# Performance work log

Hardware: AMD Instinct MI355X
Metric: run time of the kernel (lower is better)

Reference implementation:

```python
import jax, jax.numpy as jnp
import numpy as np

N_TH1 = 25
LB = 1e-20
UB = 1e20
LB_EXP = -20.0


def _make_directions(n_th1):
    # Spherical direction grid exactly as in the TF __init__ (interior ring points, then 2 poles).
    n_th2 = 2 * (n_th1 - 1) + 1
    th1 = np.linspace(-np.pi / 2, np.pi / 2, n_th1)
    th2 = np.linspace(-np.pi, np.pi, n_th2)
    c1, s1 = np.cos(th1), np.sin(th1)
    c2, s2 = np.cos(th2), np.sin(th2)
    i = np.arange(1, n_th1 - 1)
    j = np.arange(0, n_th2 - 1)
    C1 = c1[i][:, None]
    dx = (C1 * c2[j][None, :]).ravel()
    dy = (C1 * s2[j][None, :]).ravel()
    dz = np.broadcast_to(s1[i][:, None], (len(i), len(j))).ravel()
    d = np.stack([dx, dy, dz], axis=-1)
    poles = np.array([[c1[0] * c2[0], c1[0] * s2[0], s1[0]],
                      [c1[-1] * c2[0], c1[-1] * s2[0], s1[-1]]])
    return np.concatenate([d, poles], axis=0).astype(np.float32)  # [n_dirs, 3]


def setup_inputs():
    key = jax.random.key(0)
    k1, k2 = jax.random.split(key)
    B, P, V = 8, 32, 256
    vertices = jax.random.normal(k1, (B, P, V, 3), dtype=jnp.float32)
    # smoothness p in [2, 20] (power-mean exponent must be > 1 for meaningful support fn)
    smoothness = jax.random.uniform(k2, (B, P), dtype=jnp.float32) * 18.0 + 2.0
    directions = jnp.asarray(_make_directions(N_TH1))  # [1106, 3]
    return {"vertices": vertices, "smoothness": smoothness, "directions": directions}


def _forward(vertices, smoothness, directions):
    B, P, V, _ = vertices.shape
    D = directions.shape[0]
    mean_vertices = jnp.mean(vertices, axis=2, keepdims=True)          # [B,P,1,3]
    local_vertices = vertices - mean_vertices                          # [B,P,V,3]

    # z[b,p,v,d] = <local_vertex, direction>
    z = jnp.einsum('bpvc,dc->bpvd', local_vertices, directions)        # [B,P,V,D]
    zm = jnp.where(z > 0, z, 0.0)                                      # relu, == cast(z>0)*z
    p = smoothness[:, :, None, None]                                   # [B,P,1,1]

    # dynamic rescaling exponent k = 10^ceil(max(0, (-20 - p*log10(max_v zm)) / p))
    safe_zm = jnp.where(zm > 0, zm, 1.0)
    zm_log = jnp.max(jnp.where(zm > 0, jnp.log(safe_zm) / jnp.log(10.0), -jnp.inf),
                     axis=2, keepdims=True)                            # [B,P,1,D]
    exponent = zm_log * p
    lk = jnp.where(exponent < LB_EXP, (LB_EXP - exponent) / p, 0.0)
    k = jnp.power(10.0, jnp.clip(jnp.ceil(lk), 0.0, UB))               # [B,P,1,D]
    k = jax.lax.stop_gradient(k)  # ceil has zero grad in TF too

    zms = zm * k                                                       # [B,P,V,D]
    # zm^p, with exact-zero entries mapped back to 0 (clip(0^p)=LB then -LB in TF)
    safe_zms = jnp.where(zms > 0, zms, 1.0)
    zm_p = jnp.where(zms > 0, jnp.clip(jnp.power(safe_zms, p), LB, UB), 0.0)
    sum_zm_p = jnp.sum(zm_p, axis=2, keepdims=True)                    # [B,P,1,D]
    h = jnp.clip(jnp.power(sum_zm_p, 1.0 / p), LB, UB)                 # [B,P,1,D]

    # dh/dz = clip((zm_scaled / h)^(p-1)); TF keeps the LB floor here (no subtraction)
    ratio = zms / h
    safe_ratio = jnp.where(ratio > 0, ratio, 1.0)
    dhdz = jnp.where(ratio > 0, jnp.clip(jnp.power(safe_ratio, p - 1.0), LB, UB), LB)

    # surface points s = (dh/dz)^T V + t
    surf = jnp.einsum('bpvd,bpvc->bpdc', dhdz, local_vertices) + mean_vertices  # [B,P,D,3]

    h_out = jnp.transpose(h / k, (0, 1, 3, 2))                         # [B,P,D,1]
    local_dirs = jnp.broadcast_to(directions[None, None], (B, P, D, 3))
    direction_h = jnp.concatenate([local_dirs, h_out], axis=-1)        # [B,P,D,4]

    points = surf.reshape(B, P * D, 3)
    mean_v = mean_vertices.reshape(B, P, 3)
    zeros = jnp.zeros((1, 1, 1, 1), jnp.float32)
    return (points, direction_h, mean_v, directions, local_vertices, zeros, zeros)


def reference(vertices, smoothness, directions):
    return _forward(vertices, smoothness, directions)
```

## Files before the change

### kernel.cpp

```cpp
#include <hip/hip_runtime.h>
#include <math.h>

#define BLOCK 256
#define LBv 1e-20f
#define UBv 1e20f
#define LOG10_2 0.3010299956639812f

#if __has_builtin(__builtin_amdgcn_logf) && __has_builtin(__builtin_amdgcn_exp2f)
__device__ __forceinline__ float fast_log2(float x) { return __builtin_amdgcn_logf(x); }
__device__ __forceinline__ float fast_exp2(float x) { return __builtin_amdgcn_exp2f(x); }
#else
__device__ __forceinline__ float fast_log2(float x) { return log2f(x); }
__device__ __forceinline__ float fast_exp2(float x) { return exp2f(x); }
#endif

__global__ __launch_bounds__(BLOCK) void mcnet_fused(
    const float* __restrict__ verts,
    const float* __restrict__ smooth,
    const float* __restrict__ dirs,
    float* __restrict__ out,
    int NT, int V, int D, int SPLIT,
    size_t offDH, size_t offMV, size_t offDIR, size_t offLV, size_t offZ)
{
    extern __shared__ float smem[];
    float4* lv = (float4*)smem;
    float*  red = smem + 4 * (size_t)V;

    const int tid  = threadIdx.x;
    const int tile = blockIdx.x / SPLIT;
    const int s    = blockIdx.x % SPLIT;

    float sx = 0.f, sy = 0.f, sz = 0.f;
    for (int v = tid; v < V; v += BLOCK) {
        const float* vp = verts + ((size_t)tile * V + v) * 3;
        sx += vp[0]; sy += vp[1]; sz += vp[2];
    }
    red[tid] = sx; red[tid + BLOCK] = sy; red[tid + 2 * BLOCK] = sz;
    __syncthreads();
    for (int st = BLOCK / 2; st > 0; st >>= 1) {
        if (tid < st) {
            red[tid]             += red[tid + st];
            red[tid + BLOCK]     += red[tid + BLOCK + st];
            red[tid + 2 * BLOCK] += red[tid + 2 * BLOCK + st];
        }
        __syncthreads();
    }
    const float inv = 1.0f / (float)V;
    const float mx = red[0] * inv, my = red[BLOCK] * inv, mz = red[2 * BLOCK] * inv;

    for (int v = tid; v < V; v += BLOCK) {
        const float* vp = verts + ((size_t)tile * V + v) * 3;
        lv[v] = make_float4(vp[0] - mx, vp[1] - my, vp[2] - mz, 0.f);
    }
    __syncthreads();

    if (s == 0) {
        for (int v = tid; v < V; v += BLOCK) {
            float4 q = lv[v];
            size_t o = offLV + ((size_t)tile * V + v) * 3;
            out[o + 0] = q.x;
            out[o + 1] = q.y;
            out[o + 2] = q.z;
        }
        if (tid == 0) {
            size_t mo = offMV + (size_t)tile * 3;
            out[mo + 0] = mx;
            out[mo + 1] = my;
            out[mo + 2] = mz;
        }
    }
    if (blockIdx.x == 0) {
        for (int i = tid; i < D * 3; i += BLOCK)
            out[offDIR + i] = dirs[i];
        if (tid < 2) out[offZ + tid] = 0.f;
    }

    const int d = s * BLOCK + tid;
    if (d >= D) return;

    const float dx = dirs[d * 3 + 0];
    const float dy = dirs[d * 3 + 1];
    const float dz = dirs[d * 3 + 2];
    const float pv = smooth[tile];
    const float c1 = pv - 1.f;

    float zmax = 0.f, S = 0.f;
    float ax = 0.f, ay = 0.f, az = 0.f;
    #pragma unroll 8
    for (int v = 0; v < V; ++v) {
        float4 q = lv[v];
        float z  = fmaf(q.x, dx, fmaf(q.y, dy, q.z * dz));
        float zc = fmaxf(z, 0.f);
        zmax = fmaxf(zmax, zc);
        float l = fast_log2(zc);
        float w = fast_exp2(c1 * l);
        float u = w * zc;
        S += fminf(u, UBv);
        ax = fmaf(w, q.x, ax);
        ay = fmaf(w, q.y, ay);
        az = fmaf(w, q.z, az);
    }

    if (zmax > 0.f && pv * (fast_log2(zmax) * LOG10_2) >= -10.f) {
        float h = fminf(fmaxf(fast_exp2(fast_log2(S) * (1.f / pv)), LBv), UBv);
        float scale = fast_exp2(-c1 * fast_log2(h));

        size_t po = ((size_t)tile * D + d) * 3;
        out[po + 0] = fmaf(ax, scale, mx);
        out[po + 1] = fmaf(ay, scale, my);
        out[po + 2] = fmaf(az, scale, mz);

        size_t dho = offDH + ((size_t)tile * D + d) * 4;
        out[dho + 0] = dx;
        out[dho + 1] = dy;
        out[dho + 2] = dz;
        out[dho + 3] = h;
    } else {
        float zm_log   = (zmax > 0.f) ? log10f(zmax) : -INFINITY;
        float exponent = zm_log * pv;
        float lk = (exponent < -20.f) ? (-20.f - exponent) / pv : 0.f;
        float kk = powf(10.f, fminf(fmaxf(ceilf(lk), 0.f), UBv));

        float sum = 0.f;
        for (int v = 0; v < V; ++v) {
            float4 q = lv[v];
            float z   = fmaf(q.x, dx, fmaf(q.y, dy, q.z * dz));
            float zms = fmaxf(z, 0.f) * kk;
            float w   = (zms > 0.f) ? fminf(fmaxf(powf(zms, pv), LBv), UBv) : 0.f;
            sum += w;
        }
        float h = fminf(fmaxf(powf(sum, 1.f / pv), LBv), UBv);

        float bx = 0.f, by = 0.f, bz = 0.f;
        for (int v = 0; v < V; ++v) {
            float4 q = lv[v];
            float z     = fmaf(q.x, dx, fmaf(q.y, dy, q.z * dz));
            float zms   = fmaxf(z, 0.f) * kk;
            float ratio = zms / h;
            float w = (ratio > 0.f) ? fminf(fmaxf(powf(ratio, c1), LBv), UBv) : LBv;
            bx = fmaf(w, q.x, bx);
            by = fmaf(w, q.y, by);
            bz = fmaf(w, q.z, bz);
        }

        size_t po = ((size_t)tile * D + d) * 3;
        out[po + 0] = bx + mx;
        out[po + 1] = by + my;
        out[po + 2] = bz + mz;

        size_t dho = offDH + ((size_t)tile * D + d) * 4;
        out[dho + 0] = dx;
        out[dho + 1] = dy;
        out[dho + 2] = dz;
        out[dho + 3] = h / kk;
    }
}

extern "C" void kernel_launch(void* const* d_in, const int* in_sizes, int n_in,
                              void* d_out, int out_size, void* d_ws, size_t ws_size,
                              hipStream_t stream) {
    const float* verts  = (const float*)d_in[0];
    const float* smooth = (const float*)d_in[1];
    const float* dirs   = (const float*)d_in[2];
    float* out = (float*)d_out;

    const int NT = in_sizes[1];
    const int D  = in_sizes[2] / 3;
    const int V  = in_sizes[0] / (3 * NT);
    const int SPLIT = (D + BLOCK - 1) / BLOCK;

    const size_t offDH  = (size_t)NT * D * 3;
    const size_t offMV  = offDH  + (size_t)NT * D * 4;
    const size_t offDIR = offMV  + (size_t)NT * 3;
    const size_t offLV  = offDIR + (size_t)D * 3;
    const size_t offZ   = offLV  + (size_t)NT * V * 3;

    const size_t shmem = (4 * (size_t)V + 3 * BLOCK) * sizeof(float);

    dim3 grid(NT * SPLIT);
    dim3 block(BLOCK);
    hipLaunchKernelGGL(mcnet_fused, grid, block, shmem, stream,
                       verts, smooth, dirs, out,
                       NT, V, D, SPLIT, offDH, offMV, offDIR, offLV, offZ);
}
```

Before: 92.90 us.

## Process two directions per thread and drop per-vertex max tracking

Each thread now computes two directions at once, so every shared-memory vertex load is reused across both, and the grid shrinks from five splits per tile to three. The per-vertex zmax tracking and UB clamp in the hot loop are removed. The decision to take the fast path now tests the accumulated sum against a threshold, and zmax is recomputed only on the slow path. This cuts LDS traffic and instructions per direction but lowers occupancy and parallelism (fewer blocks, and the second direction idles on the last split), and the branch condition changes numerically.

Measured after the change: 97.32 us. 1.05x slower.

```diff
diff --git a/kernel.cpp b/kernel.cpp
--- a/kernel.cpp
+++ b/kernel.cpp
@@ -4,7 +4,6 @@
 #define BLOCK 256
 #define LBv 1e-20f
 #define UBv 1e20f
-#define LOG10_2 0.3010299956639812f
 
 #if __has_builtin(__builtin_amdgcn_logf) && __has_builtin(__builtin_amdgcn_exp2f)
 __device__ __forceinline__ float fast_log2(float x) { return __builtin_amdgcn_logf(x); }
@@ -14,7 +13,70 @@
 __device__ __forceinline__ float fast_exp2(float x) { return exp2f(x); }
 #endif
 
-__global__ __launch_bounds__(BLOCK) void mcnet_fused(
+__device__ __forceinline__ void finish_dir(
+    const float4* __restrict__ lv, int V, int tile, int d, int D,
+    float dx, float dy, float dz, float pv, float c1,
+    float S, float ax, float ay, float az,
+    float mx, float my, float mz, float Sthresh,
+    float* __restrict__ out, size_t offDH)
+{
+    size_t po  = ((size_t)tile * D + d) * 3;
+    size_t dho = offDH + ((size_t)tile * D + d) * 4;
+
+    if (S >= Sthresh) {
+        float h = fminf(fmaxf(fast_exp2(fast_log2(S) * (1.f / pv)), LBv), UBv);
+        float scale = fast_exp2(-c1 * fast_log2(h));
+        out[po + 0] = fmaf(ax, scale, mx);
+        out[po + 1] = fmaf(ay, scale, my);
+        out[po + 2] = fmaf(az, scale, mz);
+        out[dho + 0] = dx;
+        out[dho + 1] = dy;
+        out[dho + 2] = dz;
+        out[dho + 3] = h;
+    } else {
+        float zmax = 0.f;
+        for (int v = 0; v < V; ++v) {
+            float4 q = lv[v];
+            float z = fmaf(q.x, dx, fmaf(q.y, dy, q.z * dz));
+            zmax = fmaxf(zmax, z);
+        }
+        float zm_log   = (zmax > 0.f) ? log10f(zmax) : -INFINITY;
+        float exponent = zm_log * pv;
+        float lk = (exponent < -20.f) ? (-20.f - exponent) / pv : 0.f;
+        float kk = powf(10.f, fminf(fmaxf(ceilf(lk), 0.f), UBv));
+
+        float sum = 0.f;
+        for (int v = 0; v < V; ++v) {
+            float4 q = lv[v];
+            float z   = fmaf(q.x, dx, fmaf(q.y, dy, q.z * dz));
+            float zms = fmaxf(z, 0.f) * kk;
+            float w   = (zms > 0.f) ? fminf(fmaxf(powf(zms, pv), LBv), UBv) : 0.f;
+            sum += w;
+        }
+        float h = fminf(fmaxf(powf(sum, 1.f / pv), LBv), UBv);
+
+        float bx = 0.f, by = 0.f, bz = 0.f;
+        for (int v = 0; v < V; ++v) {
+            float4 q = lv[v];
+            float z     = fmaf(q.x, dx, fmaf(q.y, dy, q.z * dz));
+            float zms   = fmaxf(z, 0.f) * kk;
+            float ratio = zms / h;
+            float w = (ratio > 0.f) ? fminf(fmaxf(powf(ratio, c1), LBv), UBv) : LBv;
+            bx = fmaf(w, q.x, bx);
+            by = fmaf(w, q.y, by);
+            bz = fmaf(w, q.z, bz);
+        }
+        out[po + 0] = bx + mx;
+        out[po + 1] = by + my;
+        out[po + 2] = bz + mz;
+        out[dho + 0] = dx;
+        out[dho + 1] = dy;
+        out[dho + 2] = dz;
+        out[dho + 3] = h / kk;
+    }
+}
+
+__global__ __launch_bounds__(BLOCK) void mcnet_fused2(
     const float* __restrict__ verts,
     const float* __restrict__ smooth,
     const float* __restrict__ dirs,
@@ -75,85 +137,47 @@
         if (tid < 2) out[offZ + tid] = 0.f;
     }
 
-    const int d = s * BLOCK + tid;
-    if (d >= D) return;
-
-    const float dx = dirs[d * 3 + 0];
-    const float dy = dirs[d * 3 + 1];
-    const float dz = dirs[d * 3 + 2];
+    const int d0 = s * (2 * BLOCK) + tid;
+    if (d0 >= D) return;
+    const int d1 = d0 + BLOCK;
+    const bool has1 = (d1 < D);
+    const int d1c = has1 ? d1 : d0;
+
+    const float dx0 = dirs[d0 * 3 + 0], dy0 = dirs[d0 * 3 + 1], dz0 = dirs[d0 * 3 + 2];
+    const float dx1 = dirs[d1c * 3 + 0], dy1 = dirs[d1c * 3 + 1], dz1 = dirs[d1c * 3 + 2];
     const float pv = smooth[tile];
     const float c1 = pv - 1.f;
-
-    float zmax = 0.f, S = 0.f;
-    float ax = 0.f, ay = 0.f, az = 0.f;
-    #pragma unroll 8
+    const float Sthresh = (float)V * 1e-10f;
+
+    float S0 = 0.f, ax0 = 0.f, ay0 = 0.f, az0 = 0.f;
+    float S1 = 0.f, ax1 = 0.f, ay1 = 0.f, az1 = 0.f;
+
+    #pragma unroll 4
     for (int v = 0; v < V; ++v) {
         float4 q = lv[v];
-        float z  = fmaf(q.x, dx, fmaf(q.y, dy, q.z * dz));
-        float zc = fmaxf(z, 0.f);
-        zmax = fmaxf(zmax, zc);
-        float l = fast_log2(zc);
-        float w = fast_exp2(c1 * l);
-        float u = w * zc;
-        S += fminf(u, UBv);
-        ax = fmaf(w, q.x, ax);
-        ay = fmaf(w, q.y, ay);
-        az = fmaf(w, q.z, az);
-    }
-
-    if (zmax > 0.f && pv * (fast_log2(zmax) * LOG10_2) >= -10.f) {
-        float h = fminf(fmaxf(fast_exp2(fast_log2(S) * (1.f / pv)), LBv), UBv);
-        float scale = fast_exp2(-c1 * fast_log2(h));
-
-        size_t po = ((size_t)tile * D + d) * 3;
-        out[po + 0] = fmaf(ax, scale, mx);
-        out[po + 1] = fmaf(ay, scale, my);
-        out[po + 2] = fmaf(az, scale, mz);
-
-        size_t dho = offDH + ((size_t)tile * D + d) * 4;
-        out[dho + 0] = dx;
-        out[dho + 1] = dy;
-        out[dho + 2] = dz;
-        out[dho + 3] = h;
-    } else {
-        float zm_log   = (zmax > 0.f) ? log10f(zmax) : -INFINITY;
-        float exponent = zm_log * pv;
-        float lk = (exponent < -20.f) ? (-20.f - exponent) / pv : 0.f;
-        float kk = powf(10.f, fminf(fmaxf(ceilf(lk), 0.f), UBv));
-
-        float sum = 0.f;
-        for (int v = 0; v < V; ++v) {
-            float4 q = lv[v];
-            float z   = fmaf(q.x, dx, fmaf(q.y, dy, q.z * dz));
-            float zms = fmaxf(z, 0.f) * kk;
-            float w   = (zms > 0.f) ? fminf(fmaxf(powf(zms, pv), LBv), UBv) : 0.f;
-            sum += w;
-        }
-        float h = fminf(fmaxf(powf(sum, 1.f / pv), LBv), UBv);
-
-        float bx = 0.f, by = 0.f, bz = 0.f;
-        for (int v = 0; v < V; ++v) {
-            float4 q = lv[v];
-            float z     = fmaf(q.x, dx, fmaf(q.y, dy, q.z * dz));
-            float zms   = fmaxf(z, 0.f) * kk;
-            float ratio = zms / h;
-            float w = (ratio > 0.f) ? fminf(fmaxf(powf(ratio, c1), LBv), UBv) : LBv;
-            bx = fmaf(w, q.x, bx);
-            by = fmaf(w, q.y, by);
-            bz = fmaf(w, q.z, bz);
-        }
-
-        size_t po = ((size_t)tile * D + d) * 3;
-        out[po + 0] = bx + mx;
-        out[po + 1] = by + my;
-        out[po + 2] = bz + mz;
-
-        size_t dho = offDH + ((size_t)tile * D + d) * 4;
-        out[dho + 0] = dx;
-        out[dho + 1] = dy;
-        out[dho + 2] = dz;
-        out[dho + 3] = h / kk;
-    }
+        float z0 = fmaf(q.x, dx0, fmaf(q.y, dy0, q.z * dz0));
+        float z1 = fmaf(q.x, dx1, fmaf(q.y, dy1, q.z * dz1));
+        float zc0 = fmaxf(z0, 0.f);
+        float zc1 = fmaxf(z1, 0.f);
+        float l0 = fast_log2(zc0);
+        float l1 = fast_log2(zc1);
+        float w0 = fast_exp2(c1 * l0);
+        float w1 = fast_exp2(c1 * l1);
+        S0 = fmaf(w0, zc0, S0);
+        S1 = fmaf(w1, zc1, S1);
+        ax0 = fmaf(w0, q.x, ax0);
+        ay0 = fmaf(w0, q.y, ay0);
+        az0 = fmaf(w0, q.z, az0);
+        ax1 = fmaf(w1, q.x, ax1);
+        ay1 = fmaf(w1, q.y, ay1);
+        az1 = fmaf(w1, q.z, az1);
+    }
+
+    finish_dir(lv, V, tile, d0, D, dx0, dy0, dz0, pv, c1,
+               S0, ax0, ay0, az0, mx, my, mz, Sthresh, out, offDH);
+    if (has1)
+        finish_dir(lv, V, tile, d1, D, dx1, dy1, dz1, pv, c1,
+                   S1, ax1, ay1, az1, mx, my, mz, Sthresh, out, offDH);
 }
 
 extern "C" void kernel_launch(void* const* d_in, const int* in_sizes, int n_in,
@@ -167,7 +191,7 @@
     const int NT = in_sizes[1];
     const int D  = in_sizes[2] / 3;
     const int V  = in_sizes[0] / (3 * NT);
-    const int SPLIT = (D + BLOCK - 1) / BLOCK;
+    const int SPLIT = (D + 2 * BLOCK - 1) / (2 * BLOCK);
 
     const size_t offDH  = (size_t)NT * D * 3;
     const size_t offMV  = offDH  + (size_t)NT * D * 4;
@@ -179,7 +203,7 @@
 
     dim3 grid(NT * SPLIT);
     dim3 block(BLOCK);
-    hipLaunchKernelGGL(mcnet_fused, grid, block, shmem, stream,
+    hipLaunchKernelGGL(mcnet_fused2, grid, block, shmem, stream,
                        verts, smooth, dirs, out,
                        NT, V, D, SPLIT, offDH, offMV, offDIR, offLV, offZ);
 }
```

## Read vertices via uniform global loads and fold mean subtraction algebraically

Applied to the files above, without the earlier changes.

The main loop now reads raw vertices straight from global memory with block-uniform addresses, which the compiler can turn into scalar loads, instead of staging centered vertices in LDS. The mean is folded into the dot product as a constant offset, and a running weight sum Ws corrects the weighted vertex sums afterwards. The per-vertex zmax tracking and the UB clamp are dropped, and the fast-path test becomes a threshold on S instead of on zmax. This trims LDS traffic and per-iteration ALU work, at the cost of a slightly different fast/slow path criterion and possible cancellation error in the mean correction.

After: 91.80 us. Within noise of the previous version (-1.2%).

```diff
diff --git a/kernel.cpp b/kernel.cpp
--- a/kernel.cpp
+++ b/kernel.cpp
@@ -4,7 +4,6 @@
 #define BLOCK 256
 #define LBv 1e-20f
 #define UBv 1e20f
-#define LOG10_2 0.3010299956639812f
 
 #if __has_builtin(__builtin_amdgcn_logf) && __has_builtin(__builtin_amdgcn_exp2f)
 __device__ __forceinline__ float fast_log2(float x) { return __builtin_amdgcn_logf(x); }
@@ -14,7 +13,7 @@
 __device__ __forceinline__ float fast_exp2(float x) { return exp2f(x); }
 #endif
 
-__global__ __launch_bounds__(BLOCK) void mcnet_fused(
+__global__ __launch_bounds__(BLOCK) void mcnet_sreg(
     const float* __restrict__ verts,
     const float* __restrict__ smooth,
     const float* __restrict__ dirs,
@@ -22,18 +21,17 @@
     int NT, int V, int D, int SPLIT,
     size_t offDH, size_t offMV, size_t offDIR, size_t offLV, size_t offZ)
 {
-    extern __shared__ float smem[];
-    float4* lv = (float4*)smem;
-    float*  red = smem + 4 * (size_t)V;
+    __shared__ float red[3 * BLOCK];
 
     const int tid  = threadIdx.x;
     const int tile = blockIdx.x / SPLIT;
     const int s    = blockIdx.x % SPLIT;
 
+    const float* vp0 = verts + (size_t)tile * V * 3;
+
     float sx = 0.f, sy = 0.f, sz = 0.f;
     for (int v = tid; v < V; v += BLOCK) {
-        const float* vp = verts + ((size_t)tile * V + v) * 3;
-        sx += vp[0]; sy += vp[1]; sz += vp[2];
+        sx += vp0[3 * v + 0]; sy += vp0[3 * v + 1]; sz += vp0[3 * v + 2];
     }
     red[tid] = sx; red[tid + BLOCK] = sy; red[tid + 2 * BLOCK] = sz;
     __syncthreads();
@@ -48,19 +46,12 @@
     const float inv = 1.0f / (float)V;
     const float mx = red[0] * inv, my = red[BLOCK] * inv, mz = red[2 * BLOCK] * inv;
 
-    for (int v = tid; v < V; v += BLOCK) {
-        const float* vp = verts + ((size_t)tile * V + v) * 3;
-        lv[v] = make_float4(vp[0] - mx, vp[1] - my, vp[2] - mz, 0.f);
-    }
-    __syncthreads();
-
     if (s == 0) {
         for (int v = tid; v < V; v += BLOCK) {
-            float4 q = lv[v];
             size_t o = offLV + ((size_t)tile * V + v) * 3;
-            out[o + 0] = q.x;
-            out[o + 1] = q.y;
-            out[o + 2] = q.z;
+            out[o + 0] = vp0[3 * v + 0] - mx;
+            out[o + 1] = vp0[3 * v + 1] - my;
+            out[o + 2] = vp0[3 * v + 2] - mz;
         }
         if (tid == 0) {
             size_t mo = offMV + (size_t)tile * 3;
@@ -83,39 +74,50 @@
     const float dz = dirs[d * 3 + 2];
     const float pv = smooth[tile];
     const float c1 = pv - 1.f;
+    const float Sthresh = (float)V * 1e-10f;
 
-    float zmax = 0.f, S = 0.f;
-    float ax = 0.f, ay = 0.f, az = 0.f;
+    const float nmd = -(mx * dx + my * dy + mz * dz);
+
+    float S = 0.f, Wx = 0.f, Wy = 0.f, Wz = 0.f, Ws = 0.f;
     #pragma unroll 8
     for (int v = 0; v < V; ++v) {
-        float4 q = lv[v];
-        float z  = fmaf(q.x, dx, fmaf(q.y, dy, q.z * dz));
+        float vx = vp0[3 * v + 0];
+        float vy = vp0[3 * v + 1];
+        float vz = vp0[3 * v + 2];
+        float z  = fmaf(vx, dx, fmaf(vy, dy, fmaf(vz, dz, nmd)));
         float zc = fmaxf(z, 0.f);
-        zmax = fmaxf(zmax, zc);
-        float l = fast_log2(zc);
-        float w = fast_exp2(c1 * l);
-        float u = w * zc;
-        S += fminf(u, UBv);
-        ax = fmaf(w, q.x, ax);
-        ay = fmaf(w, q.y, ay);
-        az = fmaf(w, q.z, az);
+        float l  = fast_log2(zc);
+        float w  = fast_exp2(c1 * l);
+        S  = fmaf(w, zc, S);
+        Wx = fmaf(w, vx, Wx);
+        Wy = fmaf(w, vy, Wy);
+        Wz = fmaf(w, vz, Wz);
+        Ws += w;
     }
 
-    if (zmax > 0.f && pv * (fast_log2(zmax) * LOG10_2) >= -10.f) {
+    size_t po  = ((size_t)tile * D + d) * 3;
+    size_t dho = offDH + ((size_t)tile * D + d) * 4;
+
+    if (S >= Sthresh) {
         float h = fminf(fmaxf(fast_exp2(fast_log2(S) * (1.f / pv)), LBv), UBv);
         float scale = fast_exp2(-c1 * fast_log2(h));
-
-        size_t po = ((size_t)tile * D + d) * 3;
+        float ax = fmaf(-mx, Ws, Wx);
+        float ay = fmaf(-my, Ws, Wy);
+        float az = fmaf(-mz, Ws, Wz);
         out[po + 0] = fmaf(ax, scale, mx);
         out[po + 1] = fmaf(ay, scale, my);
         out[po + 2] = fmaf(az, scale, mz);
-
-        size_t dho = offDH + ((size_t)tile * D + d) * 4;
         out[dho + 0] = dx;
         out[dho + 1] = dy;
         out[dho + 2] = dz;
         out[dho + 3] = h;
     } else {
+        float zmax = 0.f;
+        for (int v = 0; v < V; ++v) {
+            float z = fmaf(vp0[3 * v] - mx, dx,
+                      fmaf(vp0[3 * v + 1] - my, dy, (vp0[3 * v + 2] - mz) * dz));
+            zmax = fmaxf(zmax, z);
+        }
         float zm_log   = (zmax > 0.f) ? log10f(zmax) : -INFINITY;
         float exponent = zm_log * pv;
         float lk = (exponent < -20.f) ? (-20.f - exponent) / pv : 0.f;
@@ -123,8 +125,8 @@
 
         float sum = 0.f;
         for (int v = 0; v < V; ++v) {
-            float4 q = lv[v];
-            float z   = fmaf(q.x, dx, fmaf(q.y, dy, q.z * dz));
+            float z = fmaf(vp0[3 * v] - mx, dx,
+                      fmaf(vp0[3 * v + 1] - my, dy, (vp0[3 * v + 2] - mz) * dz));
             float zms = fmaxf(z, 0.f) * kk;
             float w   = (zms > 0.f) ? fminf(fmaxf(powf(zms, pv), LBv), UBv) : 0.f;
             sum += w;
@@ -133,22 +135,18 @@
 
         float bx = 0.f, by = 0.f, bz = 0.f;
         for (int v = 0; v < V; ++v) {
-            float4 q = lv[v];
-            float z     = fmaf(q.x, dx, fmaf(q.y, dy, q.z * dz));
+            float lx = vp0[3 * v] - mx, ly = vp0[3 * v + 1] - my, lz = vp0[3 * v + 2] - mz;
+            float z     = fmaf(lx, dx, fmaf(ly, dy, lz * dz));
             float zms   = fmaxf(z, 0.f) * kk;
             float ratio = zms / h;
             float w = (ratio > 0.f) ? fminf(fmaxf(powf(ratio, c1), LBv), UBv) : LBv;
-            bx = fmaf(w, q.x, bx);
-            by = fmaf(w, q.y, by);
-            bz = fmaf(w, q.z, bz);
+            bx = fmaf(w, lx, bx);
+            by = fmaf(w, ly, by);
+            bz = fmaf(w, lz, bz);
         }
-
-        size_t po = ((size_t)tile * D + d) * 3;
         out[po + 0] = bx + mx;
         out[po + 1] = by + my;
         out[po + 2] = bz + mz;
-
-        size_t dho = offDH + ((size_t)tile * D + d) * 4;
         out[dho + 0] = dx;
         out[dho + 1] = dy;
         out[dho + 2] = dz;
@@ -175,11 +173,9 @@
     const size_t offLV  = offDIR + (size_t)D * 3;
     const size_t offZ   = offLV  + (size_t)NT * V * 3;
 
-    const size_t shmem = (4 * (size_t)V + 3 * BLOCK) * sizeof(float);
-
     dim3 grid(NT * SPLIT);
     dim3 block(BLOCK);
-    hipLaunchKernelGGL(mcnet_fused, grid, block, shmem, stream,
+    hipLaunchKernelGGL(mcnet_sreg, grid, block, 0, stream,
                        verts, smooth, dirs, out,
                        NT, V, D, SPLIT, offDH, offMV, offDIR, offLV, offZ);
 }
```
